# Kernel tuning notes

Hardware: AMD Instinct MI355X
Metric: run time of the kernel (lower is better)

## Reference

```python
import jax, jax.numpy as jnp
import numpy as np

SEQ, BATCH, HID, OUT = 2048, 128, 256, 2

def setup_inputs() -> dict:
    key = jax.random.key(0)
    ks = jax.random.split(key, 6)
    return {
        "x": jax.random.normal(ks[0], (SEQ, BATCH), dtype=jnp.float32),
        # torch code draws h inside forward: randn*0.01 + 0.5 -> pass as input for determinism
        "h0": jax.random.normal(ks[1], (BATCH, HID), dtype=jnp.float32) * 0.01 + 0.5,
        "W_ih": jax.random.normal(ks[2], (HID, 1), dtype=jnp.float32) * 0.05 + 0.4,
        "W_hh": jax.random.normal(ks[3], (HID, HID), dtype=jnp.float32) * 0.2,
        "W_hh_bias": jax.random.normal(ks[4], (HID, HID), dtype=jnp.float32) * 0.01 + 0.5,
        "b_h": jnp.zeros((HID,), dtype=jnp.float32),
        "W": jax.random.normal(ks[5], (OUT, HID), dtype=jnp.float32) * 0.1 + 0.5,
        "b": jnp.zeros((OUT,), dtype=jnp.float32),
        "context": 1,
    }

def reference(x, h0, W_ih, W_hh, W_hh_bias, b_h, W, b, context):
    # context is a scalar, so c1 + c2 = (2h-1) @ (W_hh + context*W_hh_bias).T (same math, one GEMM)
    W_eff = W_hh + context * W_hh_bias            # (hid, hid)
    w_in = W_ih[:, 0]                             # input_size == 1 -> (hid,)

    def step(h, x_t):
        # c0: (batch,1)@(1,hid) == outer product of x_t with W_ih column
        pre = x_t[:, None] * w_in[None, :] + (2.0 * h - 1.0) @ W_eff.T + b_h
        h_new = jax.nn.sigmoid(pre)
        return h_new, h_new

    _, hs = jax.lax.scan(step, h0, x)             # hs: (seq, batch, hid)
    out = jnp.transpose(hs, (1, 0, 2))            # (batch, seq, hid)
    y = out @ W.T + b                             # (batch, seq, out)
    return y[:, :, 0], out
```

## Files before the change

### kernel.cpp

```cpp
#include <hip/hip_runtime.h>
#include <math.h>

#define SEQ   2048
#define BATCH 128
#define HID   256
#define NCH   16
#define KCH   16
#define VST   20

template <int CTRL>
__device__ __forceinline__ float dpp_mov(float x) {
    return __int_as_float(__builtin_amdgcn_update_dpp(
        __float_as_int(x), __float_as_int(x), CTRL, 0xF, 0xF, false));
}

__global__ __launch_bounds__(512) __attribute__((amdgpu_waves_per_eu(2, 2)))
void rnn_scan_kernel(const float* __restrict__ x,
                     const float* __restrict__ h0,
                     const float* __restrict__ W_ih,
                     const float* __restrict__ W_hh,
                     const float* __restrict__ W_hh_b,
                     const float* __restrict__ b_h,
                     const int*   __restrict__ context,
                     const float* __restrict__ Wout,
                     const float* __restrict__ bias,
                     float*       __restrict__ out_hs,
                     float*       __restrict__ out_y)
{
    const int b   = blockIdx.x;
    const int tid = threadIdx.x;
    const int R   = tid >> 4;
    const int l   = tid & 15;
    const int l7  = tid & 7;
    const int row = 8 * R + l7;

    __shared__ __align__(16) float v_lds[2][NCH * VST];
    __shared__ float x_lds[SEQ];

    for (int t = tid; t < SEQ; t += 512)
        x_lds[t] = x[t * BATCH + b];

    const float ctx = (float)context[0];

    float4 wreg[8][4];
    #pragma unroll
    for (int j = 0; j < 8; ++j) {
        const int rj = 8 * R + (l7 ^ j);
        const float* wp = W_hh   + (size_t)rj * HID + KCH * l;
        const float* bp = W_hh_b + (size_t)rj * HID + KCH * l;
        #pragma unroll
        for (int c = 0; c < 4; ++c) {
            const float4 a = *(const float4*)(wp + 4 * c);
            const float4 d = *(const float4*)(bp + 4 * c);
            wreg[j][c] = make_float4(a.x + ctx * d.x, a.y + ctx * d.y,
                                     a.z + ctx * d.z, a.w + ctx * d.w);
        }
    }

    const float winj = W_ih[row];
    const float bhj  = b_h[row];

    const int voff = VST * (row >> 4) + (row & 15);
    v_lds[0][voff] = 2.f * h0[(size_t)b * HID + row] - 1.f;

    float* outp = out_hs + (size_t)b * SEQ * HID + row;

    const float4* vr0 = (const float4*)(v_lds[0] + VST * l);
    const float4* vr1 = (const float4*)(v_lds[1] + VST * l);

    __syncthreads();

    auto step = [&](int t, const float4* __restrict__ vr, float* __restrict__ vw) {
        const float xt = x_lds[t];
        float q[8] = {0.f, 0.f, 0.f, 0.f, 0.f, 0.f, 0.f, 0.f};
        #pragma unroll
        for (int c = 0; c < 4; ++c) {
            const float4 v4 = vr[c];
            #pragma unroll
            for (int j = 0; j < 8; ++j) {
                const float4 w = wreg[j][c];
                q[j] += w.x * v4.x;
                q[j] += w.y * v4.y;
                q[j] += w.z * v4.z;
                q[j] += w.w * v4.w;
            }
        }
        #pragma unroll
        for (int j = 0; j < 8; ++j) q[j] += dpp_mov<0x128>(q[j]);
        q[0] += dpp_mov<0xB1>(q[1]);
        q[2] += dpp_mov<0xB1>(q[3]);
        q[4] += dpp_mov<0xB1>(q[5]);
        q[6] += dpp_mov<0xB1>(q[7]);
        q[0] += dpp_mov<0x4E>(q[2]);
        q[4] += dpp_mov<0x4E>(q[6]);
        q[0] += dpp_mov<0x124>(q[4]);

        const float pre = q[0] + bhj + xt * winj;
        const float h = 1.f / (1.f + __expf(-pre));
        vw[voff] = 2.f * h - 1.f;
        if ((tid & 8) == 0)
            outp[(size_t)t * HID] = h;
        __syncthreads();
    };

    for (int t = 0; t < SEQ; t += 2) {
        step(t,     vr0, v_lds[1]);
        step(t + 1, vr1, v_lds[0]);
    }

    __threadfence();
    __syncthreads();

    {
        const int sub  = tid & 15;
        const int rsub = tid >> 4;
        float4 w0[4];
        #pragma unroll
        for (int u = 0; u < 4; ++u)
            w0[u] = *(const float4*)(Wout + 4 * (16 * u + sub));
        const float b0 = bias[0];
        const float* hsb = out_hs + (size_t)b * SEQ * HID;
        float* yp = out_y + (size_t)b * SEQ;

        for (int r0 = 0; r0 < SEQ; r0 += 32) {
            const int t = r0 + rsub;
            const float* rp = hsb + (size_t)t * HID;
            float s = 0.f;
            #pragma unroll
            for (int u = 0; u < 4; ++u) {
                const float4 hv = *(const float4*)(rp + 4 * (16 * u + sub));
                s += hv.x * w0[u].x + hv.y * w0[u].y +
                     hv.z * w0[u].z + hv.w * w0[u].w;
            }
            s += __shfl_xor(s, 1, 64);
            s += __shfl_xor(s, 2, 64);
            s += __shfl_xor(s, 4, 64);
            s += __shfl_xor(s, 8, 64);
            if (sub == 0) yp[t] = s + b0;
        }
    }
}

extern "C" void kernel_launch(void* const* d_in, const int* in_sizes, int n_in,
                              void* d_out, int out_size, void* d_ws, size_t ws_size,
                              hipStream_t stream) {
    const float* x      = (const float*)d_in[0];
    const float* h0     = (const float*)d_in[1];
    const float* W_ih   = (const float*)d_in[2];
    const float* W_hh   = (const float*)d_in[3];
    const float* W_hh_b = (const float*)d_in[4];
    const float* b_h    = (const float*)d_in[5];
    const float* W      = (const float*)d_in[6];
    const float* bias   = (const float*)d_in[7];
    const int*   ctx    = (const int*)d_in[8];

    float* y  = (float*)d_out;
    float* hs = y + (size_t)BATCH * SEQ;

    rnn_scan_kernel<<<BATCH, 512, 0, stream>>>(x, h0, W_ih, W_hh, W_hh_b,
                                               b_h, ctx, W, bias, hs, y);
}
```

Before: 1.404 ms.

## Compute recurrent matvec with split-fp16 MFMA instead of fp32 FMA with DPP reduction

Replaces the per-thread fp32 FMA dot products and DPP cross-lane reductions with 16x16x32 fp16 MFMA instructions. Weights and the hidden-state vector are each split into high and low fp16 parts, and four MFMAs per tile recover near-fp32 accuracy. The state vector is stored in LDS as fp16 hi/lo arrays. This trades fewer scalar FMAs and shuffles for four MFMA passes that issue back to back on a latency-bound serial chain, with some risk to precision and to step latency.

After: 2.869 ms. 104% more time.

```diff
diff --git a/kernel.cpp b/kernel.cpp
--- a/kernel.cpp
+++ b/kernel.cpp
@@ -4,17 +4,13 @@
 #define SEQ   2048
 #define BATCH 128
 #define HID   256
-#define NCH   16
-#define KCH   16
-#define VST   20
 
-template <int CTRL>
-__device__ __forceinline__ float dpp_mov(float x) {
-    return __int_as_float(__builtin_amdgcn_update_dpp(
-        __float_as_int(x), __float_as_int(x), CTRL, 0xF, 0xF, false));
-}
+typedef _Float16 f16;
+typedef _Float16 f16x8 __attribute__((ext_vector_type(8)));
+typedef _Float16 f16x4 __attribute__((ext_vector_type(4)));
+typedef float    f32x4 __attribute__((ext_vector_type(4)));
 
-__global__ __launch_bounds__(512) __attribute__((amdgpu_waves_per_eu(2, 2)))
+__global__ __launch_bounds__(512, 2)
 void rnn_scan_kernel(const float* __restrict__ x,
                      const float* __restrict__ h0,
                      const float* __restrict__ W_ih,
@@ -27,14 +23,17 @@
                      float*       __restrict__ out_hs,
                      float*       __restrict__ out_y)
 {
-    const int b   = blockIdx.x;
-    const int tid = threadIdx.x;
-    const int R   = tid >> 4;
-    const int l   = tid & 15;
-    const int l7  = tid & 7;
-    const int row = 8 * R + l7;
+    const int b    = blockIdx.x;
+    const int tid  = threadIdx.x;
+    const int w    = tid >> 6;
+    const int lane = tid & 63;
+    const int n    = lane & 15;
+    const int g    = lane >> 4;
+    const int mi_s = n >> 3;
+    const int q    = n & 7;
 
-    __shared__ __align__(16) float v_lds[2][NCH * VST];
+    __shared__ __align__(16) f16 Vh[2][HID];
+    __shared__ __align__(16) f16 Vl[2][HID];
     __shared__ float x_lds[SEQ];
 
     for (int t = tid; t < SEQ; t += 512)
@@ -42,75 +41,101 @@
 
     const float ctx = (float)context[0];
 
-    float4 wreg[8][4];
+    f16x8 Ah[2][8], Al[2][8];
     #pragma unroll
-    for (int j = 0; j < 8; ++j) {
-        const int rj = 8 * R + (l7 ^ j);
-        const float* wp = W_hh   + (size_t)rj * HID + KCH * l;
-        const float* bp = W_hh_b + (size_t)rj * HID + KCH * l;
+    for (int mi = 0; mi < 2; ++mi) {
+        const int m = 2 * w + mi;
+        const float* wp = W_hh   + (size_t)(16 * m + n) * HID;
+        const float* bp = W_hh_b + (size_t)(16 * m + n) * HID;
         #pragma unroll
-        for (int c = 0; c < 4; ++c) {
-            const float4 a = *(const float4*)(wp + 4 * c);
-            const float4 d = *(const float4*)(bp + 4 * c);
-            wreg[j][c] = make_float4(a.x + ctx * d.x, a.y + ctx * d.y,
-                                     a.z + ctx * d.z, a.w + ctx * d.w);
+        for (int kt = 0; kt < 8; ++kt) {
+            const int c0 = 32 * kt + 8 * g;
+            f16x8 hv, lv;
+            #pragma unroll
+            for (int e = 0; e < 8; ++e) {
+                const float we = wp[c0 + e] + ctx * bp[c0 + e];
+                const f16 wh = (f16)we;
+                hv[e] = wh;
+                lv[e] = (f16)(we - (float)wh);
+            }
+            Ah[mi][kt] = hv;
+            Al[mi][kt] = lv;
         }
     }
 
-    const float winj = W_ih[row];
-    const float bhj  = b_h[row];
+    const int rowbase = 16 * (2 * w + mi_s) + 4 * g;
+    float bh4[4], win4[4];
+    #pragma unroll
+    for (int r = 0; r < 4; ++r) {
+        bh4[r]  = b_h[rowbase + r];
+        win4[r] = W_ih[rowbase + r];
+    }
 
-    const int voff = VST * (row >> 4) + (row & 15);
-    v_lds[0][voff] = 2.f * h0[(size_t)b * HID + row] - 1.f;
+    if (tid < HID) {
+        const float v  = 2.f * h0[(size_t)b * HID + tid] - 1.f;
+        const f16   vh = (f16)v;
+        Vh[0][tid] = vh;
+        Vl[0][tid] = (f16)(v - (float)vh);
+    }
 
-    float* outp = out_hs + (size_t)b * SEQ * HID + row;
-
-    const float4* vr0 = (const float4*)(v_lds[0] + VST * l);
-    const float4* vr1 = (const float4*)(v_lds[1] + VST * l);
+    float* outp = out_hs + (size_t)b * SEQ * HID;
 
     __syncthreads();
 
-    auto step = [&](int t, const float4* __restrict__ vr, float* __restrict__ vw) {
+    auto step = [&](int t, const f16* __restrict__ vhr, const f16* __restrict__ vlr,
+                    f16* __restrict__ vhw, f16* __restrict__ vlw) {
         const float xt = x_lds[t];
-        float q[8] = {0.f, 0.f, 0.f, 0.f, 0.f, 0.f, 0.f, 0.f};
+
+        const f32x4 z = {0.f, 0.f, 0.f, 0.f};
+        f32x4 acc[2][2] = {{z, z}, {z, z}};
         #pragma unroll
-        for (int c = 0; c < 4; ++c) {
-            const float4 v4 = vr[c];
+        for (int kt = 0; kt < 8; ++kt) {
+            const f16x8 bh = *(const f16x8*)(vhr + 32 * kt + 8 * g);
+            const f16x8 bl = *(const f16x8*)(vlr + 32 * kt + 8 * g);
+            const int p = kt & 1;
             #pragma unroll
-            for (int j = 0; j < 8; ++j) {
-                const float4 w = wreg[j][c];
-                q[j] += w.x * v4.x;
-                q[j] += w.y * v4.y;
-                q[j] += w.z * v4.z;
-                q[j] += w.w * v4.w;
+            for (int mi = 0; mi < 2; ++mi) {
+                acc[mi][p] = __builtin_amdgcn_mfma_f32_16x16x32_f16(Ah[mi][kt], bh, acc[mi][p], 0, 0, 0);
+                acc[mi][p] = __builtin_amdgcn_mfma_f32_16x16x32_f16(Ah[mi][kt], bl, acc[mi][p], 0, 0, 0);
+                acc[mi][p] = __builtin_amdgcn_mfma_f32_16x16x32_f16(Al[mi][kt], bh, acc[mi][p], 0, 0, 0);
+                acc[mi][p] = __builtin_amdgcn_mfma_f32_16x16x32_f16(Al[mi][kt], bl, acc[mi][p], 0, 0, 0);
             }
         }
+
+        float h0r, h1r, h2r, h3r;
+        f16x4 vhp, vlp;
         #pragma unroll
-        for (int j = 0; j < 8; ++j) q[j] += dpp_mov<0x128>(q[j]);
-        q[0] += dpp_mov<0xB1>(q[1]);
-        q[2] += dpp_mov<0xB1>(q[3]);
-        q[4] += dpp_mov<0xB1>(q[5]);
-        q[6] += dpp_mov<0xB1>(q[7]);
-        q[0] += dpp_mov<0x4E>(q[2]);
-        q[4] += dpp_mov<0x4E>(q[6]);
-        q[0] += dpp_mov<0x124>(q[4]);
+        for (int r = 0; r < 4; ++r) {
+            const float s0 = acc[0][0][r] + acc[0][1][r];
+            const float s1 = acc[1][0][r] + acc[1][1][r];
+            const float pre = (mi_s ? s1 : s0) + bh4[r] + xt * win4[r];
+            const float h = 1.f / (1.f + __expf(-pre));
+            if (r == 0) h0r = h; else if (r == 1) h1r = h;
+            else if (r == 2) h2r = h; else h3r = h;
+            const float v  = 2.f * h - 1.f;
+            const f16   vh = (f16)v;
+            vhp[r] = vh;
+            vlp[r] = (f16)(v - (float)vh);
+        }
 
-        const float pre = q[0] + bhj + xt * winj;
-        const float h = 1.f / (1.f + __expf(-pre));
-        vw[voff] = 2.f * h - 1.f;
-        if ((tid & 8) == 0)
-            outp[(size_t)t * HID] = h;
+        if (q == 0) {
+            *(f16x4*)(vhw + rowbase) = vhp;
+            *(f16x4*)(vlw + rowbase) = vlp;
+        }
+        if (q < 4) {
+            const float hq = (q == 0) ? h0r : (q == 1) ? h1r : (q == 2) ? h2r : h3r;
+            outp[(size_t)t * HID + rowbase + q] = hq;
+        }
         __syncthreads();
     };
 
     for (int t = 0; t < SEQ; t += 2) {
-        step(t,     vr0, v_lds[1]);
-        step(t + 1, vr1, v_lds[0]);
+        step(t,     Vh[0], Vl[0], Vh[1], Vl[1]);
+        step(t + 1, Vh[1], Vl[1], Vh[0], Vl[0]);
     }
 
     __threadfence();
     __syncthreads();
-
     {
         const int sub  = tid & 15;
         const int rsub = tid >> 4;
```
